# Kernel tuning notes

Measured on AMD Instinct MI355X. Metric: run time of the kernel, lower is better.

The kernel has to match this reference:

```python
import jax, jax.numpy as jnp
import numpy as np

N, K, CIN, COUT = 1_000_000, 27, 32, 32  # active voxels, 3^3 kernel offsets, channels
EPS = 1e-5


def setup_inputs() -> dict:
    key = jax.random.key(0)
    k0, k1, k2, k3 = jax.random.split(key, 4)
    feats = jax.random.normal(k0, (N, CIN), jnp.float32)
    # per-kernel-offset weight matrices, Kaiming-ish scale
    W = jax.random.normal(k1, (K, CIN, COUT), jnp.float32) * (1.0 / np.sqrt(K * CIN))
    gamma = jnp.ones((COUT,), jnp.float32)
    beta = jnp.zeros((COUT,), jnp.float32)
    # precomputed sparse-conv neighbor map: index of input voxel contributing
    nbr_idx = jax.random.randint(k2, (N, K), 0, N, jnp.int32)
    nbr_mask = jax.random.bernoulli(k3, 0.5, (N, K))
    return {"feats": feats, "W": W, "gamma": gamma, "beta": beta,
            "nbr_idx": nbr_idx, "nbr_mask": nbr_mask}


def _sparse_conv(feats, W, nbr_idx, nbr_mask):
    # gather-GEMM-scatter, looped over the small fixed kernel volume (27)
    # to avoid materializing an [N, 27, CIN] gathered tensor.
    acc = jnp.zeros((feats.shape[0], W.shape[2]), feats.dtype)
    for k in range(W.shape[0]):
        g = jnp.where(nbr_mask[:, k, None], feats[nbr_idx[:, k]], 0.0)  # [N, CIN]
        acc = acc + g @ W[k]  # [N, COUT]
    return acc


def reference(feats, W, gamma, beta, nbr_idx, nbr_mask):
    y = _sparse_conv(feats, W, nbr_idx, nbr_mask)           # conv (bias=False, bn=True)
    mean = jnp.mean(y, axis=0)                              # MinkowskiBatchNorm (batch stats)
    var = jnp.mean(jnp.square(y - mean), axis=0)
    y = (y - mean) * jax.lax.rsqrt(var + EPS) * gamma + beta
    return jax.nn.relu(y)                                   # MinkowskiReLU
```

## Files before the change

kernel.cpp:

```cpp
#include <hip/hip_runtime.h>

typedef _Float16 half8 __attribute__((ext_vector_type(8)));
typedef float floatx4 __attribute__((ext_vector_type(4)));

#define CIN 32
#define COUT 32
#define KOFF 27
#define EPSV 1e-5f


__global__ void setup_k(const float* __restrict__ W, _Float16* __restrict__ wp,
                        const unsigned char* __restrict__ m,
                        int* __restrict__ flag) {
  if (blockIdx.x < KOFF) {
    int ko = blockIdx.x;
    int h = threadIdx.x >> 6;
    int lane = threadIdx.x & 63;
    int col = lane & 15, quad = lane >> 4;
    half8 p;
#pragma unroll
    for (int j = 0; j < 8; ++j) {
      int k = quad * 8 + j;
      p[j] = (_Float16)W[(ko * CIN + k) * COUT + h * 16 + col];
    }
    *(half8*)(wp + ((size_t)(ko * 2 + h) * 64 + lane) * 8) = p;
  } else {
    int tid = threadIdx.x;
    int any = 0;
    for (int i = tid; i < 4096; i += 128) {
      if ((i & 3) != 0 && m[i] != 0) any = 1;
    }
    if (any) atomicOr(flag, 1);
  }
}

__global__ void prep_k(const float* __restrict__ feats,
                       _Float16* __restrict__ f16, int total8,
                       const int* __restrict__ nidx,
                       const unsigned char* __restrict__ nmask,
                       const int* __restrict__ flagp,
                       int* __restrict__ nbrT, int N, int cvtBlocks) {
  __shared__ int lds[256 * 29];
  int tid = threadIdx.x;
  if ((int)blockIdx.x < cvtBlocks) {
    int t = blockIdx.x * 256 + tid;
    if (t >= total8) return;
    const floatx4* in4 = (const floatx4*)feats;
    floatx4 a = __builtin_nontemporal_load(&in4[t * 2]);
    floatx4 b = __builtin_nontemporal_load(&in4[t * 2 + 1]);
    half8 h;
    h[0] = (_Float16)a[0]; h[1] = (_Float16)a[1];
    h[2] = (_Float16)a[2]; h[3] = (_Float16)a[3];
    h[4] = (_Float16)b[0]; h[5] = (_Float16)b[1];
    h[6] = (_Float16)b[2]; h[7] = (_Float16)b[3];
    *(half8*)(f16 + (size_t)t * 8) = h;
  } else {
    bool bytemode = (*flagp != 0);
    const int* nmask32 = (const int*)nmask;
    int tileBase = (blockIdx.x - cvtBlocks) * 256;
    int nvox = min(256, N - tileBase);
    if (nvox <= 0) return;
    int total = nvox * KOFF;
    for (int p = tid; p < total; p += 256) {
      int voxl = p / KOFF;
      int ko = p - voxl * KOFF;
      int g = tileBase * KOFF + p;
      int idx = __builtin_nontemporal_load(&nidx[g]);
      int mk = bytemode ? (int)__builtin_nontemporal_load(&nmask[g])
                        : __builtin_nontemporal_load(&nmask32[g]);
      lds[voxl * 29 + ko] = (idx & 0x7FFFFFFF) | (mk ? (int)0x80000000 : 0);
    }
    __syncthreads();
    if (tid < nvox) {
#pragma unroll
      for (int ko = 0; ko < KOFF; ++ko) {
        __builtin_nontemporal_store(lds[tid * 29 + ko],
                                    &nbrT[(size_t)ko * N + tileBase + tid]);
      }
    }
  }
}

__launch_bounds__(256)
__global__ void conv_mfma_t(const _Float16* __restrict__ f16,
                            const _Float16* __restrict__ wp,
                            const int* __restrict__ nbrT,
                            float* __restrict__ y,
                            float* __restrict__ stats, int N) {
  __shared__ float smS[4 * 32];
  __shared__ float smQ[4 * 32];
  int wave = threadIdx.x >> 6;
  int lane = threadIdx.x & 63;
  int base = (blockIdx.x * 4 + wave) * 64;
  bool active = base < N;
  int col = lane & 15, quad = lane >> 4;
  const half8* wfrag = (const half8*)wp;

  floatx4 acc[4][2];
#pragma unroll
  for (int t = 0; t < 4; ++t)
#pragma unroll
    for (int h = 0; h < 2; ++h) {
      acc[t][h][0] = 0.f; acc[t][h][1] = 0.f;
      acc[t][h][2] = 0.f; acc[t][h][3] = 0.f;
    }

  if (active) {
    int vcur[4];
#pragma unroll
    for (int t = 0; t < 4; ++t)
      vcur[t] = __builtin_nontemporal_load(&nbrT[(size_t)base + t * 16 + col]);

#pragma unroll 3
    for (int ko = 0; ko < KOFF; ++ko) {
      int vnext[4] = {0, 0, 0, 0};
      if (ko + 1 < KOFF) {
#pragma unroll
        for (int t = 0; t < 4; ++t)
          vnext[t] = __builtin_nontemporal_load(
              &nbrT[(size_t)(ko + 1) * N + base + t * 16 + col]);
      }
      half8 b0 = wfrag[(size_t)(ko * 2 + 0) * 64 + lane];
      half8 b1 = wfrag[(size_t)(ko * 2 + 1) * 64 + lane];
#pragma unroll
      for (int t = 0; t < 4; ++t) {
        half8 a;
#pragma unroll
        for (int j = 0; j < 8; ++j) a[j] = (_Float16)0.f;
        if (vcur[t] < 0) {
          int nb = vcur[t] & 0x7FFFFFFF;
          a = *(const half8*)(f16 + (size_t)nb * CIN + quad * 8);
        }
        acc[t][0] = __builtin_amdgcn_mfma_f32_16x16x32_f16(a, b0, acc[t][0], 0, 0, 0);
        acc[t][1] = __builtin_amdgcn_mfma_f32_16x16x32_f16(a, b1, acc[t][1], 0, 0, 0);
      }
#pragma unroll
      for (int t = 0; t < 4; ++t) vcur[t] = vnext[t];
    }
  }

  float s0 = 0.f, s1 = 0.f, q0 = 0.f, q1 = 0.f;
  if (active) {
#pragma unroll
    for (int t = 0; t < 4; ++t) {
#pragma unroll
      for (int h = 0; h < 2; ++h) {
        floatx4 c = acc[t][h];
        int co = h * 16 + col;
#pragma unroll
        for (int r = 0; r < 4; ++r) {
          int vox = base + t * 16 + quad * 4 + r;
          y[(size_t)vox * COUT + co] = c[r];
          float v = c[r];
          if (h == 0) { s0 += v; q0 += v * v; }
          else        { s1 += v; q1 += v * v; }
        }
      }
    }
  }
  s0 += __shfl_xor(s0, 16); s0 += __shfl_xor(s0, 32);
  s1 += __shfl_xor(s1, 16); s1 += __shfl_xor(s1, 32);
  q0 += __shfl_xor(q0, 16); q0 += __shfl_xor(q0, 32);
  q1 += __shfl_xor(q1, 16); q1 += __shfl_xor(q1, 32);
  if (quad == 0) {
    smS[wave * 32 + col] = s0;
    smS[wave * 32 + 16 + col] = s1;
    smQ[wave * 32 + col] = q0;
    smQ[wave * 32 + 16 + col] = q1;
  }
  __syncthreads();
  int tid = threadIdx.x;
  if (tid < 64) {
    int co = tid & 31;
    const float* arr = (tid < 32) ? smS : smQ;
    float s = arr[co] + arr[32 + co] + arr[64 + co] + arr[96 + co];
    atomicAdd(&stats[(tid < 32 ? 0 : 32) + co], s);
  }
}

__global__ void bn_apply(float* __restrict__ y, const float* __restrict__ stats,
                         const float* __restrict__ gamma,
                         const float* __restrict__ beta, int total4, float invN) {
  __shared__ float sc_sh[64];
  int tid = threadIdx.x;
  if (tid < 32) {
    float mean = stats[tid] * invN;
    float ex2 = stats[32 + tid] * invN;
    float var = ex2 - mean * mean;
    float inv = rsqrtf(var + EPSV);
    float sc = gamma[tid] * inv;
    sc_sh[tid] = sc;
    sc_sh[32 + tid] = beta[tid] - mean * sc;
  }
  __syncthreads();
  int t = blockIdx.x * blockDim.x + tid;
  if (t >= total4) return;
  size_t g = (size_t)t * 4;
  int co = (int)(g & 31);
  floatx4 v = *(const floatx4*)(y + g);
  floatx4 sc = *(const floatx4*)&sc_sh[co];
  floatx4 sh = *(const floatx4*)&sc_sh[32 + co];
  floatx4 o;
#pragma unroll
  for (int j = 0; j < 4; ++j) o[j] = fmaxf(0.f, v[j] * sc[j] + sh[j]);
  __builtin_nontemporal_store(o, (floatx4*)(y + g));
}

extern "C" void kernel_launch(void* const* d_in, const int* in_sizes, int n_in,
                              void* d_out, int out_size, void* d_ws,
                              size_t ws_size, hipStream_t stream) {
  const float* feats = (const float*)d_in[0];
  const float* W = (const float*)d_in[1];
  const float* gamma = (const float*)d_in[2];
  const float* beta = (const float*)d_in[3];
  const int* nidx = (const int*)d_in[4];
  const unsigned char* nmask = (const unsigned char*)d_in[5];
  float* out = (float*)d_out;

  int N = in_sizes[0] / CIN;

  char* ws = (char*)d_ws;
  size_t f16_bytes = (size_t)N * CIN * sizeof(_Float16);
  _Float16* f16 = (_Float16*)ws;
  _Float16* wp = (_Float16*)(ws + f16_bytes);
  size_t wp_bytes = (size_t)KOFF * 2 * 64 * 8 * sizeof(_Float16);
  size_t stats_off = ((f16_bytes + wp_bytes + 511) / 512) * 512;
  float* stats = (float*)(ws + stats_off);
  int* flag = (int*)(stats + 64);
  size_t nbrT_off = ((stats_off + 768 + 255) / 256) * 256;
  int* nbrT = (int*)(ws + nbrT_off);

  hipMemsetAsync(stats, 0, 65 * sizeof(float), stream);

  setup_k<<<KOFF + 1, 128, 0, stream>>>(W, wp, nmask, flag);

  int total8 = N * CIN / 8;
  int cvtBlocks = (total8 + 255) / 256;
  int nbrBlocks = (N + 255) / 256;
  prep_k<<<cvtBlocks + nbrBlocks, 256, 0, stream>>>(feats, f16, total8, nidx,
                                                    nmask, flag, nbrT, N,
                                                    cvtBlocks);

  int nwaves = (N + 63) / 64;
  int nblocks = (nwaves + 3) / 4;
  conv_mfma_t<<<nblocks, 256, 0, stream>>>(f16, wp, nbrT, out, stats, N);

  int total4 = N * COUT / 4;
  bn_apply<<<(total4 + 255) / 256, 256, 0, stream>>>(out, stats, gamma, beta,
                                                     total4, 1.0f / (float)N);
}
```

Before: 731.1 us.

## Drop neighbor-index transpose, pack mask bits, read nidx directly with branchless gathers

Removes the prep pass that transposed nbr_idx and mask into a [27,N] packed array. Instead each voxel's 27 mask flags are packed into one 32-bit word, and the conv kernel reads nidx in its original row-major layout. Masked neighbors are redirected to an appended zero row of the fp16 feature buffer, which makes the gather branchless. The conv loop is fully unrolled and software-pipelined, prefetching indices two offsets ahead and features and weights one offset ahead, with launch bounds raised to ask for three blocks per SIMD. This avoids writing and re-reading a 108MB transposed index array, at the cost of strided per-lane nidx reads and higher register pressure.

```diff
diff --git a/kernel.cpp b/kernel.cpp
--- a/kernel.cpp
+++ b/kernel.cpp
@@ -36,55 +36,53 @@
 
 __global__ void prep_k(const float* __restrict__ feats,
                        _Float16* __restrict__ f16, int total8,
-                       const int* __restrict__ nidx,
                        const unsigned char* __restrict__ nmask,
                        const int* __restrict__ flagp,
-                       int* __restrict__ nbrT, int N, int cvtBlocks) {
-  __shared__ int lds[256 * 29];
+                       unsigned int* __restrict__ mpack, int N,
+                       int cvtBlocks) {
   int tid = threadIdx.x;
   if ((int)blockIdx.x < cvtBlocks) {
     int t = blockIdx.x * 256 + tid;
-    if (t >= total8) return;
-    const floatx4* in4 = (const floatx4*)feats;
-    floatx4 a = __builtin_nontemporal_load(&in4[t * 2]);
-    floatx4 b = __builtin_nontemporal_load(&in4[t * 2 + 1]);
-    half8 h;
-    h[0] = (_Float16)a[0]; h[1] = (_Float16)a[1];
-    h[2] = (_Float16)a[2]; h[3] = (_Float16)a[3];
-    h[4] = (_Float16)b[0]; h[5] = (_Float16)b[1];
-    h[6] = (_Float16)b[2]; h[7] = (_Float16)b[3];
-    *(half8*)(f16 + (size_t)t * 8) = h;
+    if (t < total8) {
+      const floatx4* in4 = (const floatx4*)feats;
+      floatx4 a = __builtin_nontemporal_load(&in4[(size_t)t * 2]);
+      floatx4 b = __builtin_nontemporal_load(&in4[(size_t)t * 2 + 1]);
+      half8 h;
+      h[0] = (_Float16)a[0]; h[1] = (_Float16)a[1];
+      h[2] = (_Float16)a[2]; h[3] = (_Float16)a[3];
+      h[4] = (_Float16)b[0]; h[5] = (_Float16)b[1];
+      h[6] = (_Float16)b[2]; h[7] = (_Float16)b[3];
+      *(half8*)(f16 + (size_t)t * 8) = h;
+    } else if (t < total8 + 4) {
+      half8 z;
+#pragma unroll
+      for (int j = 0; j < 8; ++j) z[j] = (_Float16)0.f;
+      *(half8*)(f16 + (size_t)t * 8) = z;
+    }
   } else {
-    bool bytemode = (*flagp != 0);
-    const int* nmask32 = (const int*)nmask;
-    int tileBase = (blockIdx.x - cvtBlocks) * 256;
-    int nvox = min(256, N - tileBase);
-    if (nvox <= 0) return;
-    int total = nvox * KOFF;
-    for (int p = tid; p < total; p += 256) {
-      int voxl = p / KOFF;
-      int ko = p - voxl * KOFF;
-      int g = tileBase * KOFF + p;
-      int idx = __builtin_nontemporal_load(&nidx[g]);
-      int mk = bytemode ? (int)__builtin_nontemporal_load(&nmask[g])
-                        : __builtin_nontemporal_load(&nmask32[g]);
-      lds[voxl * 29 + ko] = (idx & 0x7FFFFFFF) | (mk ? (int)0x80000000 : 0);
-    }
-    __syncthreads();
-    if (tid < nvox) {
-#pragma unroll
-      for (int ko = 0; ko < KOFF; ++ko) {
-        __builtin_nontemporal_store(lds[tid * 29 + ko],
-                                    &nbrT[(size_t)ko * N + tileBase + tid]);
-      }
-    }
-  }
-}
-
-__launch_bounds__(256)
-__global__ void conv_mfma_t(const _Float16* __restrict__ f16,
+    int vox = (blockIdx.x - cvtBlocks) * 256 + tid;
+    if (vox >= N) return;
+    unsigned int mk = 0;
+    if (*flagp != 0) {
+      const unsigned char* p = nmask + (size_t)vox * KOFF;
+#pragma unroll
+      for (int ko = 0; ko < KOFF; ++ko)
+        mk |= (p[ko] != 0 ? 1u : 0u) << ko;
+    } else {
+      const int* p = (const int*)nmask + (size_t)vox * KOFF;
+#pragma unroll
+      for (int ko = 0; ko < KOFF; ++ko)
+        mk |= (p[ko] != 0 ? 1u : 0u) << ko;
+    }
+    mpack[vox] = mk;
+  }
+}
+
+__launch_bounds__(256, 3)
+__global__ void conv_mfma_d(const _Float16* __restrict__ f16,
                             const _Float16* __restrict__ wp,
-                            const int* __restrict__ nbrT,
+                            const int* __restrict__ nidx,
+                            const unsigned int* __restrict__ mpack,
                             float* __restrict__ y,
                             float* __restrict__ stats, int N) {
   __shared__ float smS[4 * 32];
@@ -95,6 +93,7 @@
   bool active = base < N;
   int col = lane & 15, quad = lane >> 4;
   const half8* wfrag = (const half8*)wp;
+  const _Float16* fq = f16 + quad * 8;
 
   floatx4 acc[4][2];
 #pragma unroll
@@ -106,36 +105,62 @@
     }
 
   if (active) {
-    int vcur[4];
-#pragma unroll
-    for (int t = 0; t < 4; ++t)
-      vcur[t] = __builtin_nontemporal_load(&nbrT[(size_t)base + t * 16 + col]);
-
-#pragma unroll 3
+    unsigned int mp[4];
+    int o27[4];
+#pragma unroll
+    for (int t = 0; t < 4; ++t) {
+      int vox = base + t * 16 + col;
+      if (vox > N - 1) vox = N - 1;
+      o27[t] = vox * KOFF;
+      mp[t] = mpack[vox];
+    }
+    int ivB[4];
+    half8 aC[4];
+#pragma unroll
+    for (int t = 0; t < 4; ++t) {
+      int iv0 = nidx[o27[t]];
+      int sel = (mp[t] & 1u) ? iv0 : N;
+      aC[t] = *(const half8*)(fq + ((size_t)sel << 5));
+    }
+#pragma unroll
+    for (int t = 0; t < 4; ++t) ivB[t] = nidx[o27[t] + 1];
+    half8 bC0 = wfrag[lane];
+    half8 bC1 = wfrag[64 + lane];
+
+#pragma unroll
     for (int ko = 0; ko < KOFF; ++ko) {
-      int vnext[4] = {0, 0, 0, 0};
+      int ivN[4];
+      if (ko + 2 < KOFF) {
+#pragma unroll
+        for (int t = 0; t < 4; ++t) ivN[t] = nidx[o27[t] + ko + 2];
+      }
+      half8 bN0, bN1;
       if (ko + 1 < KOFF) {
-#pragma unroll
-        for (int t = 0; t < 4; ++t)
-          vnext[t] = __builtin_nontemporal_load(
-              &nbrT[(size_t)(ko + 1) * N + base + t * 16 + col]);
-      }
-      half8 b0 = wfrag[(size_t)(ko * 2 + 0) * 64 + lane];
-      half8 b1 = wfrag[(size_t)(ko * 2 + 1) * 64 + lane];
+        bN0 = wfrag[(size_t)((ko + 1) * 2 + 0) * 64 + lane];
+        bN1 = wfrag[(size_t)((ko + 1) * 2 + 1) * 64 + lane];
+      }
+      half8 aN[4];
+      if (ko + 1 < KOFF) {
+#pragma unroll
+        for (int t = 0; t < 4; ++t) {
+          int sel = ((mp[t] >> (ko + 1)) & 1u) ? ivB[t] : N;
+          aN[t] = *(const half8*)(fq + ((size_t)sel << 5));
+        }
+      }
 #pragma unroll
       for (int t = 0; t < 4; ++t) {
-        half8 a;
-#pragma unroll
-        for (int j = 0; j < 8; ++j) a[j] = (_Float16)0.f;
-        if (vcur[t] < 0) {
-          int nb = vcur[t] & 0x7FFFFFFF;
-          a = *(const half8*)(f16 + (size_t)nb * CIN + quad * 8);
-        }
-        acc[t][0] = __builtin_amdgcn_mfma_f32_16x16x32_f16(a, b0, acc[t][0], 0, 0, 0);
-        acc[t][1] = __builtin_amdgcn_mfma_f32_16x16x32_f16(a, b1, acc[t][1], 0, 0, 0);
-      }
-#pragma unroll
-      for (int t = 0; t < 4; ++t) vcur[t] = vnext[t];
+        acc[t][0] = __builtin_amdgcn_mfma_f32_16x16x32_f16(aC[t], bC0, acc[t][0], 0, 0, 0);
+        acc[t][1] = __builtin_amdgcn_mfma_f32_16x16x32_f16(aC[t], bC1, acc[t][1], 0, 0, 0);
+      }
+      if (ko + 1 < KOFF) {
+#pragma unroll
+        for (int t = 0; t < 4; ++t) aC[t] = aN[t];
+        bC0 = bN0; bC1 = bN1;
+      }
+      if (ko + 2 < KOFF) {
+#pragma unroll
+        for (int t = 0; t < 4; ++t) ivB[t] = ivN[t];
+      }
     }
   }
 
@@ -150,10 +175,12 @@
 #pragma unroll
         for (int r = 0; r < 4; ++r) {
           int vox = base + t * 16 + quad * 4 + r;
-          y[(size_t)vox * COUT + co] = c[r];
-          float v = c[r];
-          if (h == 0) { s0 += v; q0 += v * v; }
-          else        { s1 += v; q1 += v * v; }
+          if (vox < N) {
+            y[(size_t)vox * COUT + co] = c[r];
+            float v = c[r];
+            if (h == 0) { s0 += v; q0 += v * v; }
+            else        { s1 += v; q1 += v * v; }
+          }
         }
       }
     }
@@ -220,30 +247,29 @@
   int N = in_sizes[0] / CIN;
 
   char* ws = (char*)d_ws;
-  size_t f16_bytes = (size_t)N * CIN * sizeof(_Float16);
+  size_t f16_bytes = (size_t)(N + 1) * CIN * sizeof(_Float16);
   _Float16* f16 = (_Float16*)ws;
   _Float16* wp = (_Float16*)(ws + f16_bytes);
   size_t wp_bytes = (size_t)KOFF * 2 * 64 * 8 * sizeof(_Float16);
   size_t stats_off = ((f16_bytes + wp_bytes + 511) / 512) * 512;
   float* stats = (float*)(ws + stats_off);
   int* flag = (int*)(stats + 64);
-  size_t nbrT_off = ((stats_off + 768 + 255) / 256) * 256;
-  int* nbrT = (int*)(ws + nbrT_off);
+  size_t mpack_off = ((stats_off + 768 + 255) / 256) * 256;
+  unsigned int* mpack = (unsigned int*)(ws + mpack_off);
 
   hipMemsetAsync(stats, 0, 65 * sizeof(float), stream);
 
   setup_k<<<KOFF + 1, 128, 0, stream>>>(W, wp, nmask, flag);
 
   int total8 = N * CIN / 8;
-  int cvtBlocks = (total8 + 255) / 256;
-  int nbrBlocks = (N + 255) / 256;
-  prep_k<<<cvtBlocks + nbrBlocks, 256, 0, stream>>>(feats, f16, total8, nidx,
-                                                    nmask, flag, nbrT, N,
-                                                    cvtBlocks);
+  int cvtBlocks = (total8 + 4 + 255) / 256;
+  int mkBlocks = (N + 255) / 256;
+  prep_k<<<cvtBlocks + mkBlocks, 256, 0, stream>>>(feats, f16, total8, nmask,
+                                                   flag, mpack, N, cvtBlocks);
 
   int nwaves = (N + 63) / 64;
   int nblocks = (nwaves + 3) / 4;
-  conv_mfma_t<<<nblocks, 256, 0, stream>>>(f16, wp, nbrT, out, stats, N);
+  conv_mfma_d<<<nblocks, 256, 0, stream>>>(f16, wp, nidx, mpack, out, stats, N);
 
   int total4 = N * COUT / 4;
   bn_apply<<<(total4 + 255) / 256, 256, 0, stream>>>(out, stats, gamma, beta,
```

Result: faster. 683.3 us (-6.5%).
